# Kernel tuning notes

Measured on AMD Instinct MI355X. Metric: run time of the kernel, lower is better.

The kernel has to match this reference:

```python
import jax, jax.numpy as jnp
import numpy as np
from jax import lax

NS, C_IN, C_FEAT, CROP = 16, 3, 32, 256


def _conv(x, w, b):
    # 3x3 stride-1 'SAME' conv == padding=1 in torch
    y = lax.conv_general_dilated(x, w, (1, 1), 'SAME',
                                 dimension_numbers=('NCHW', 'OIHW', 'NCHW'))
    return y + b[None, :, None, None]


def _lrn(x, size=5, alpha=1e-4, beta=0.75, k=1.0):
    # PyTorch LocalResponseNorm: x / (k + alpha/size * sum_window x^2)^beta
    pad = size // 2
    sq = jnp.pad(x * x, ((0, 0), (pad, pad), (0, 0), (0, 0)))
    c = x.shape[1]
    win = sum(sq[:, i:i + c] for i in range(size))
    return x / (k + (alpha / size) * win) ** beta


def setup_inputs() -> dict:
    key = jax.random.key(0)
    ks = jax.random.split(key, 6)
    s = 0.05
    h = np.hanning(CROP).astype(np.float32)
    cos_window = jnp.asarray(np.outer(h, h))
    return {
        'z': jax.random.normal(ks[0], (NS, C_IN, CROP, CROP), jnp.float32),
        'w1': jax.random.normal(ks[1], (C_FEAT, C_IN, 3, 3), jnp.float32) * s,
        'b1': jax.random.normal(ks[2], (C_FEAT,), jnp.float32) * s,
        'w2': jax.random.normal(ks[3], (C_FEAT, C_FEAT, 3, 3), jnp.float32) * s,
        'b2': jax.random.normal(ks[4], (C_FEAT,), jnp.float32) * s,
        'cos_window': cos_window,
        'wf': jax.random.normal(ks[5], (1, C_FEAT, CROP, CROP // 2 + 1, 2), jnp.float32) * s,
    }


def reference(z, w1, b1, w2, b2, cos_window, wf):
    # feature extractor: conv -> relu -> conv -> LRN
    f = jax.nn.relu(_conv(z, w1, b1))
    f = _lrn(_conv(f, w2, b2))
    f = f * cos_window  # (ns, 32, crop, crop)
    zf = jnp.fft.rfft2(f, axes=(-2, -1))  # (ns, 32, crop, crop//2+1) complex
    # faithful to source: w_star = conj(wf), and the loop always uses w_star[0, 1]
    # (fixed channel 1) multiplied with zf[c, l], accumulated over l. wf is detached.
    wc = lax.stop_gradient(wf[0, 1, :, :, 0] - 1j * wf[0, 1, :, :, 1])
    ftrans = wc[None, None] * jnp.sum(zf, axis=1, keepdims=True)  # (ns,1,crop,crop//2+1)
    response = jnp.fft.irfft2(ftrans, s=(CROP, CROP), axes=(-2, -1))
    return response  # (ns, 1, crop, crop)
```

## Files before the change

kernel.cpp:

```cpp
#include <hip/hip_runtime.h>
#include <math.h>

#define NS   16
#define CIN  3
#define CF   32
#define CROP 256
#define KH   129

typedef _Float16 half8  __attribute__((ext_vector_type(8)));
typedef _Float16 half4v __attribute__((ext_vector_type(4)));
typedef _Float16 half2v __attribute__((ext_vector_type(2)));
typedef float    f32x4  __attribute__((ext_vector_type(4)));
typedef unsigned int u32x4 __attribute__((ext_vector_type(4)));

__device__ __forceinline__ half8 neg8(half8 v) {
    u32x4 u = __builtin_bit_cast(u32x4, v);
    u ^= (u32x4){0x80008000u, 0x80008000u, 0x80008000u, 0x80008000u};
    return __builtin_bit_cast(half8, u);
}

__device__ __forceinline__ int swz8(int b, int nb) {
    int q = nb >> 3, r = nb & 7;
    int x = b & 7, o = b >> 3;
    return (x < r ? x * (q + 1) : r * (q + 1) + (x - r) * q) + o;
}

#define X_OFF 0
#define Z_OFF 21504
#define LDS_BYTES 23904

__device__ __forceinline__ int xaddr(int q, int s) {
    return X_OFF + (q << 6) + ((s ^ ((q >> 1) & 3)) << 4);
}

__device__ __forceinline__ int pi_of(int co) {
    int h = co >> 3, j = co & 7;
    return (j < 4) ? (h * 4 + j) : (16 + h * 4 + j - 4);
}
__device__ __forceinline__ int cinv_of(int p) {
    int h = (p & 15) >> 2;
    int j = (p & 3) + ((p >= 16) ? 4 : 0);
    return h * 8 + j;
}

__device__ __forceinline__ void split_pair(float v0, float v1,
                                           half2v* hp, half2v* lp) {
    _Float16 h0 = (_Float16)v0, h1 = (_Float16)v1;
    *hp = (half2v){h0, h1};
    *lp = (half2v){(_Float16)(v0 - (float)h0), (_Float16)(v1 - (float)h1)};
}

__global__ __launch_bounds__(256)
void prep(const float* __restrict__ w1, const float* __restrict__ w2,
          _Float16* __restrict__ w1pk, _Float16* __restrict__ w2lin,
          _Float16* __restrict__ TAh, _Float16* __restrict__ TAl,
          _Float16* __restrict__ G1h, _Float16* __restrict__ G1l,
          _Float16* __restrict__ G3h, _Float16* __restrict__ G3l,
          _Float16* __restrict__ TCh, _Float16* __restrict__ TCl)
{
    const int bid = blockIdx.x, tid = threadIdx.x;

    if (bid >= 134) {
        int base = (bid - 134) * 4096;
        #pragma unroll
        for (int i = 0; i < 16; ++i) {
            int e = base + tid + i * 256;
            if (e < 9216) {
                int co = e / 288;
                int r  = e - co * 288;
                int ci = r / 9, k9 = r - ci * 9;
                w2lin[(k9 * 32 + pi_of(co)) * 32 + ci] = (_Float16)w2[e];
            } else if (e < 9344) {
                int t = e - 9216;
                int lane = t & 63;
                int p = (t >> 6) * 16 + (lane & 15);
                int c = cinv_of(p);
                #pragma unroll
                for (int j = 0; j < 8; ++j) {
                    int k = ((lane >> 4) << 3) + j;
                    w1pk[t * 8 + j] = (k < 27) ? (_Float16)w1[c * 27 + k]
                                               : (_Float16)0.f;
                }
            }
        }
        return;
    }

    __shared__ float cs[256], sn[256];
    {
        float s, c;
        sincosf(0.02454369260617025967f * (float)tid, &s, &c);
        cs[tid] = c; sn[tid] = s;
    }
    __syncthreads();

    if (bid < 34) {
        int base = bid * 1024 + tid;
        #pragma unroll
        for (int i = 0; i < 4; ++i) {
            int p = base + i * 256;
            int j0 = (p & 3) * 2, lane = (p >> 2) & 63, q = p >> 8;
            int nt = q % 17, ks = q / 17;
            int x0 = ks * 32 + ((lane >> 4) << 3) + j0;
            int c = nt * 16 + (lane & 15);
            float v0 = 0.f, v1 = 0.f;
            if (c <= 128) {
                v0 =  cs[(x0 * c) & 255];
                v1 =  cs[((x0 + 1) * c) & 255];
            } else if (c >= 136 && c <= 264) {
                int cc = c - 136;
                v0 = -sn[(x0 * cc) & 255];
                v1 = -sn[((x0 + 1) * cc) & 255];
            }
            half2v hv, lv; split_pair(v0, v1, &hv, &lv);
            ((half2v*)TAh)[p] = hv; ((half2v*)TAl)[p] = lv;
        }
    } else if (bid < 98) {
        int base = (bid - 34) * 1024 + tid;
        #pragma unroll
        for (int i = 0; i < 4; ++i) {
            int p = base + i * 256;
            int j0 = (p & 3) * 2, lane = (p >> 2) & 63, q = p >> 8;
            int nt = q & 15, ks = q >> 4;
            int kk0 = ks * 32 + ((lane >> 4) << 3) + j0;
            int m  = nt * 16 + (lane & 15);
            int part = kk0 >> 8;
            int y0 = kk0 & 255;
            int i0 = (y0 * m) & 255, i1 = ((y0 + 1) * m) & 255;
            float cv0 = cs[i0], s0 = sn[i0], cv1 = cs[i1], s1 = sn[i1];
            half2v hv, lv;
            float a0 = part ? s0 : cv0,  a1 = part ? s1 : cv1;
            split_pair(a0, a1, &hv, &lv);
            ((half2v*)G1h)[p] = hv; ((half2v*)G1l)[p] = lv;
            a0 = (part ? -s0 : cv0) * (1.f/256.f);
            a1 = (part ? -s1 : cv1) * (1.f/256.f);
            split_pair(a0, a1, &hv, &lv);
            ((half2v*)G3h)[p] = hv; ((half2v*)G3l)[p] = lv;
        }
    } else {
        int base = (bid - 98) * 1024 + tid;
        #pragma unroll
        for (int i = 0; i < 4; ++i) {
            int p = base + i * 256;
            int j0 = (p & 3) * 2, lane = (p >> 2) & 63, q = p >> 8;
            int nt = q & 15, ks = q >> 4;
            int kk0 = ks * 32 + ((lane >> 4) << 3) + j0;
            int x  = nt * 16 + (lane & 15);
            int part = (kk0 >= 144) ? 1 : 0;
            int k0 = kk0 - part * 144;
            float v0 = 0.f, v1 = 0.f;
            if (k0 <= 128) {
                float w0 = (k0 == 0 || k0 == 128) ? 1.f : 2.f;
                int ii = (k0 * x) & 255;
                v0 = (part ? -w0 * sn[ii] : w0 * cs[ii]) * (1.f/256.f);
            }
            int k1 = k0 + 1;
            if (k1 <= 128) {
                float w1w = (k1 == 0 || k1 == 128) ? 1.f : 2.f;
                int ii = (k1 * x) & 255;
                v1 = (part ? -w1w * sn[ii] : w1w * cs[ii]) * (1.f/256.f);
            }
            half2v hv, lv; split_pair(v0, v1, &hv, &lv);
            ((half2v*)TCh)[p] = hv; ((half2v*)TCl)[p] = lv;
        }
    }
}

__global__ __launch_bounds__(256, 5)
void fused_features(const float* __restrict__ z,
                    const _Float16* __restrict__ w1pk,
                    const float* __restrict__ b1,
                    const _Float16* __restrict__ w2lin,
                    const float* __restrict__ b2,
                    const float* __restrict__ cosw,
                    _Float16* __restrict__ g2h, _Float16* __restrict__ g2l)
{
    __shared__ __align__(16) unsigned char smem[LDS_BYTES];
    _Float16* ztile = (_Float16*)(smem + Z_OFF);

    const int tid  = threadIdx.x;
    const int lane = tid & 63;
    const int wv   = tid >> 6;
    const int l15  = lane & 15;
    const int lhi  = lane >> 4;

    const int n  = blockIdx.z;
    const int bx = blockIdx.x, by = blockIdx.y;
    const int fy0 = by * 16 - 1;
    const int fx0 = bx * 16 - 1;

    const int zy0 = by * 16 - 2;
    const int zx0 = bx * 16 - 2;
    for (int idx = tid; idx < CIN * 400; idx += 256) {
        int ci = idx / 400;
        int r  = idx - ci * 400;
        int yy = r / 20, xx = r - yy * 20;
        int gy = zy0 + yy, gx = zx0 + xx;
        float v = 0.0f;
        if ((unsigned)gy < CROP && (unsigned)gx < CROP)
            v = z[((n * CIN + ci) * CROP + gy) * CROP + gx];
        ztile[idx] = (_Float16)v;
    }

    half8 w1f0 = *(const half8*)(w1pk + lane * 8);
    half8 w1f1 = *(const half8*)(w1pk + 512 + lane * 8);
    float bias1v[2][4], bias2v[2][4];
    #pragma unroll
    for (int cg = 0; cg < 2; ++cg)
        #pragma unroll
        for (int r = 0; r < 4; ++r) {
            bias1v[cg][r] = b1[8 * lhi + 4 * cg + r];
            bias2v[cg][r] = b2[8 * lhi + 4 * cg + r];
        }

    int offs[8];
    #pragma unroll
    for (int j = 0; j < 8; ++j) {
        int k = lhi * 8 + j;
        int ci = k / 9, rr = k - ci * 9;
        int ky = rr / 3, kx = rr - ky * 3;
        offs[j] = (k < 27) ? (ci * 400 + ky * 20 + kx) : 0;
    }
    __syncthreads();

    const f32x4 zero4 = {0.f, 0.f, 0.f, 0.f};
    for (int t = wv; t < 21; t += 4) {
        int qp = t * 16 + l15;
        int qpc = qp < 324 ? qp : 323;
        int y = qpc / 18, x = qpc - y * 18;
        const _Float16* zb = ztile + y * 20 + x;
        half8 bfrag;
        #pragma unroll
        for (int j = 0; j < 8; ++j) bfrag[j] = zb[offs[j]];
        f32x4 d0 = __builtin_amdgcn_mfma_f32_16x16x32_f16(w1f0, bfrag, zero4, 0, 0, 0);
        f32x4 d1 = __builtin_amdgcn_mfma_f32_16x16x32_f16(w1f1, bfrag, zero4, 0, 0, 0);
        int gy = fy0 + y, gx = fx0 + x;
        bool ok = ((unsigned)gy < CROP) && ((unsigned)gx < CROP) && (qp < 324);
        half8 o8;
        #pragma unroll
        for (int r = 0; r < 4; ++r) {
            float v0 = ok ? fmaxf(d0[r] + bias1v[0][r], 0.f) : 0.f;
            float v1 = ok ? fmaxf(d1[r] + bias1v[1][r], 0.f) : 0.f;
            o8[r]     = (_Float16)v0;
            o8[4 + r] = (_Float16)v1;
        }
        *(half8*)(smem + xaddr(qp, lhi)) = o8;
    }
    __syncthreads();

    f32x4 acc[4][2];
    #pragma unroll
    for (int tt = 0; tt < 4; ++tt)
        #pragma unroll
        for (int cg = 0; cg < 2; ++cg)
            #pragma unroll
            for (int r = 0; r < 4; ++r)
                acc[tt][cg][r] = bias2v[cg][r];

    #pragma unroll
    for (int k9 = 0; k9 < 9; ++k9) {
        const int ky = k9 / 3, kx = k9 - 3 * ky;
        half8 af0 = *(const half8*)(w2lin + (k9 * 32 + l15)      * 32 + lhi * 8);
        half8 af1 = *(const half8*)(w2lin + (k9 * 32 + l15 + 16) * 32 + lhi * 8);
        #pragma unroll
        for (int tt = 0; tt < 4; ++tt) {
            int q = (wv * 4 + tt + ky) * 18 + l15 + kx;
            half8 bf = *(const half8*)(smem + xaddr(q, lhi));
            acc[tt][0] = __builtin_amdgcn_mfma_f32_16x16x32_f16(af0, bf, acc[tt][0], 0, 0, 0);
            acc[tt][1] = __builtin_amdgcn_mfma_f32_16x16x32_f16(af1, bf, acc[tt][1], 0, 0, 0);
        }
    }

    const bool bot = (lhi == 0), top = (lhi == 3);
    #pragma unroll
    for (int tt = 0; tt < 4; ++tt) {
        float aA0 = acc[tt][0][0], aA1 = acc[tt][0][1],
              aA2 = acc[tt][0][2], aA3 = acc[tt][0][3];
        float aB0 = acc[tt][1][0], aB1 = acc[tt][1][1],
              aB2 = acc[tt][1][2], aB3 = acc[tt][1][3];
        float sA0 = aA0 * aA0, sA1 = aA1 * aA1, sA2 = aA2 * aA2, sA3 = aA3 * aA3;
        float sB0 = aB0 * aB0, sB1 = aB1 * aB1, sB2 = aB2 * aB2, sB3 = aB3 * aB3;
        int up = (lane + 16) & 63, dn = (lane + 48) & 63;
        float em2 = __shfl(sB2, dn); em2 = bot ? 0.f : em2;
        float em1 = __shfl(sB3, dn); em1 = bot ? 0.f : em1;
        float ep8 = __shfl(sA0, up); ep8 = top ? 0.f : ep8;
        float ep9 = __shfl(sA1, up); ep9 = top ? 0.f : ep9;
        float s = 0.f, win = em2 + em1 + sA0 + sA1 + sA2;
        float t2, f;
        t2 = 2e-5f * win; f = fmaf(t2, fmaf(t2, 0.65625f, -0.75f), 1.0f);
        s = fmaf(aA0, f, s);  win += sA3 - em2;
        t2 = 2e-5f * win; f = fmaf(t2, fmaf(t2, 0.65625f, -0.75f), 1.0f);
        s = fmaf(aA1, f, s);  win += sB0 - em1;
        t2 = 2e-5f * win; f = fmaf(t2, fmaf(t2, 0.65625f, -0.75f), 1.0f);
        s = fmaf(aA2, f, s);  win += sB1 - sA0;
        t2 = 2e-5f * win; f = fmaf(t2, fmaf(t2, 0.65625f, -0.75f), 1.0f);
        s = fmaf(aA3, f, s);  win += sB2 - sA1;
        t2 = 2e-5f * win; f = fmaf(t2, fmaf(t2, 0.65625f, -0.75f), 1.0f);
        s = fmaf(aB0, f, s);  win += sB3 - sA2;
        t2 = 2e-5f * win; f = fmaf(t2, fmaf(t2, 0.65625f, -0.75f), 1.0f);
        s = fmaf(aB1, f, s);  win += ep8 - sA3;
        t2 = 2e-5f * win; f = fmaf(t2, fmaf(t2, 0.65625f, -0.75f), 1.0f);
        s = fmaf(aB2, f, s);  win += ep9 - sB0;
        t2 = 2e-5f * win; f = fmaf(t2, fmaf(t2, 0.65625f, -0.75f), 1.0f);
        s = fmaf(aB3, f, s);
        s += __shfl_xor(s, 16);
        s += __shfl_xor(s, 32);
        if (lhi == 0) {
            int gy = by * 16 + wv * 4 + tt, gx = bx * 16 + l15;
            float val = s * cosw[gy * CROP + gx];
            _Float16 h = (_Float16)val;
            int o = (n * CROP + gy) * CROP + gx;
            g2h[o] = h;
            g2l[o] = (_Float16)(val - (float)h);
        }
    }
}

__global__ __launch_bounds__(256, 4)
void fft_rows(const _Float16* __restrict__ g2h, const _Float16* __restrict__ g2l,
              const _Float16* __restrict__ TAh, const _Float16* __restrict__ TAl,
              _Float16* __restrict__ Zth, _Float16* __restrict__ Ztl)
{
    const int lane = threadIdx.x & 63;
    const int bsw = swz8(blockIdx.x, 1088);
    const int wu = bsw * 4 + (threadIdx.x >> 6);
    const int mt = wu / 17, nt = wu - mt * 17;
    const int l15 = lane & 15, lhi = lane >> 4;
    const int rowA = mt * 16 + l15;

    f32x4 a0 = {}, a1 = {}, a2 = {};
    #pragma unroll
    for (int ks = 0; ks < 8; ++ks) {
        const int ao = rowA * 256 + ks * 32 + lhi * 8;
        half8 Ah = *(const half8*)(g2h + ao);
        half8 Al = *(const half8*)(g2l + ao);
        const int bo = ((ks * 17 + nt) * 64 + lane) * 8;
        half8 Bh = *(const half8*)(TAh + bo);
        half8 Bl = *(const half8*)(TAl + bo);
        a0 = __builtin_amdgcn_mfma_f32_16x16x32_f16(Ah, Bh, a0, 0, 0, 0);
        a1 = __builtin_amdgcn_mfma_f32_16x16x32_f16(Ah, Bl, a1, 0, 0, 0);
        a2 = __builtin_amdgcn_mfma_f32_16x16x32_f16(Al, Bh, a2, 0, 0, 0);
    }
    f32x4 acc;
    #pragma unroll
    for (int r = 0; r < 4; ++r) acc[r] = a0[r] + a1[r] + a2[r];

    const int rowD = mt * 16 + lhi * 4;
    const int n = rowD >> 8, y = rowD & 255;
    int c = nt * 16 + l15;
    int row_k = -1, koff = 0;
    if (c <= 128)                  { row_k = c;       koff = 0;   }
    else if (c >= 136 && c <= 264) { row_k = c - 136; koff = 256; }
    if (row_k >= 0) {
        half4v hv, lv;
        #pragma unroll
        for (int r = 0; r < 4; ++r) {
            float v = acc[r];
            _Float16 h = (_Float16)v;
            hv[r] = h; lv[r] = (_Float16)(v - (float)h);
        }
        size_t o = (size_t)(n * 129 + row_k) * 512 + koff + y;
        *(half4v*)(Zth + o) = hv;
        *(half4v*)(Ztl + o) = lv;
    }
}

__global__ __launch_bounds__(256, 2)
void fft_cols_mul(const _Float16* __restrict__ Zth, const _Float16* __restrict__ Ztl,
                  const _Float16* __restrict__ G1h, const _Float16* __restrict__ G1l,
                  const float* __restrict__ wf,
                  _Float16* __restrict__ Ph, _Float16* __restrict__ Pl)
{
    const int lane = threadIdx.x & 63;
    const int bsw = swz8(blockIdx.x, 516);
    const int wu = bsw * 4 + (threadIdx.x >> 6);
    const int mt = wu >> 4, nt = wu & 15;
    const int l15 = lane & 15, lhi = lane >> 4;
    const int rowA = mt * 16 + l15;

    f32x4 r0 = {}, r1 = {}, r2 = {}, i0 = {}, i1 = {}, i2 = {};
    #pragma unroll
    for (int ks = 0; ks < 8; ++ks) {
        const int ao0 = rowA * 512 + ks * 32 + lhi * 8;
        half8 Ah0 = *(const half8*)(Zth + ao0);
        half8 Al0 = *(const half8*)(Ztl + ao0);
        half8 Ah1 = *(const half8*)(Zth + ao0 + 256);
        half8 Al1 = *(const half8*)(Ztl + ao0 + 256);
        const int bo0 = ((ks * 16 + nt) * 64 + lane) * 8;
        half8 B0h = *(const half8*)(G1h + bo0);
        half8 B0l = *(const half8*)(G1l + bo0);
        half8 B1h_ = *(const half8*)(G1h + bo0 + 65536);
        half8 B1l_ = *(const half8*)(G1l + bo0 + 65536);
        half8 nB1h = neg8(B1h_), nB1l = neg8(B1l_);
        r0 = __builtin_amdgcn_mfma_f32_16x16x32_f16(Ah0, B0h,  r0, 0, 0, 0);
        r1 = __builtin_amdgcn_mfma_f32_16x16x32_f16(Ah0, B0l,  r1, 0, 0, 0);
        r2 = __builtin_amdgcn_mfma_f32_16x16x32_f16(Al0, B0h,  r2, 0, 0, 0);
        r0 = __builtin_amdgcn_mfma_f32_16x16x32_f16(Ah1, B1h_, r0, 0, 0, 0);
        r1 = __builtin_amdgcn_mfma_f32_16x16x32_f16(Ah1, B1l_, r1, 0, 0, 0);
        r2 = __builtin_amdgcn_mfma_f32_16x16x32_f16(Al1, B1h_, r2, 0, 0, 0);
        i0 = __builtin_amdgcn_mfma_f32_16x16x32_f16(Ah0, nB1h, i0, 0, 0, 0);
        i1 = __builtin_amdgcn_mfma_f32_16x16x32_f16(Ah0, nB1l, i1, 0, 0, 0);
        i2 = __builtin_amdgcn_mfma_f32_16x16x32_f16(Al0, nB1h, i2, 0, 0, 0);
        i0 = __builtin_amdgcn_mfma_f32_16x16x32_f16(Ah1, B0h,  i0, 0, 0, 0);
        i1 = __builtin_amdgcn_mfma_f32_16x16x32_f16(Ah1, B0l,  i1, 0, 0, 0);
        i2 = __builtin_amdgcn_mfma_f32_16x16x32_f16(Al1, B0h,  i2, 0, 0, 0);
    }
    const int rowP0 = mt * 16 + lhi * 4;
    const int m = nt * 16 + l15;
    const float* wf1 = wf + 256 * 129 * 2;
    int n_ = rowP0 / 129;
    int k_ = rowP0 - n_ * 129;
    #pragma unroll
    for (int r = 0; r < 4; ++r) {
        float wr = wf1[(m * 129 + k_) * 2 + 0];
        float wi = wf1[(m * 129 + k_) * 2 + 1];
        float fr = r0[r] + r1[r] + r2[r];
        float fi = i0[r] + i1[r] + i2[r];
        float pr = wr * fr + wi * fi;
        float pi = wr * fi - wi * fr;
        size_t o = (size_t)(rowP0 + r) * 512 + m;
        _Float16 h;
        h = (_Float16)pr; Ph[o] = h;       Pl[o] = (_Float16)(pr - (float)h);
        h = (_Float16)pi; Ph[o + 256] = h; Pl[o + 256] = (_Float16)(pi - (float)h);
        if (++k_ == 129) { k_ = 0; ++n_; }
    }
}

__global__ __launch_bounds__(256, 2)
void fft_cols_inv(const _Float16* __restrict__ Ph, const _Float16* __restrict__ Pl,
                  const _Float16* __restrict__ G3h, const _Float16* __restrict__ G3l,
                  _Float16* __restrict__ Bth, _Float16* __restrict__ Btl)
{
    const int lane = threadIdx.x & 63;
    const int bsw = swz8(blockIdx.x, 516);
    const int wu = bsw * 4 + (threadIdx.x >> 6);
    const int mt = wu >> 4, nt = wu & 15;
    const int l15 = lane & 15, lhi = lane >> 4;
    const int rowA = mt * 16 + l15;

    f32x4 r0 = {}, r1 = {}, r2 = {}, i0 = {}, i1 = {}, i2 = {};
    #pragma unroll
    for (int ks = 0; ks < 8; ++ks) {
        const int ao0 = rowA * 512 + ks * 32 + lhi * 8;
        half8 Ah0 = *(const half8*)(Ph + ao0);
        half8 Al0 = *(const half8*)(Pl + ao0);
        half8 Ah1 = *(const half8*)(Ph + ao0 + 256);
        half8 Al1 = *(const half8*)(Pl + ao0 + 256);
        const int bo0 = ((ks * 16 + nt) * 64 + lane) * 8;
        half8 B0h = *(const half8*)(G3h + bo0);
        half8 B0l = *(const half8*)(G3l + bo0);
        half8 B1h_ = *(const half8*)(G3h + bo0 + 65536);
        half8 B1l_ = *(const half8*)(G3l + bo0 + 65536);
        half8 nB1h = neg8(B1h_), nB1l = neg8(B1l_);
        r0 = __builtin_amdgcn_mfma_f32_16x16x32_f16(Ah0, B0h,  r0, 0, 0, 0);
        r1 = __builtin_amdgcn_mfma_f32_16x16x32_f16(Ah0, B0l,  r1, 0, 0, 0);
        r2 = __builtin_amdgcn_mfma_f32_16x16x32_f16(Al0, B0h,  r2, 0, 0, 0);
        r0 = __builtin_amdgcn_mfma_f32_16x16x32_f16(Ah1, B1h_, r0, 0, 0, 0);
        r1 = __builtin_amdgcn_mfma_f32_16x16x32_f16(Ah1, B1l_, r1, 0, 0, 0);
        r2 = __builtin_amdgcn_mfma_f32_16x16x32_f16(Al1, B1h_, r2, 0, 0, 0);
        i0 = __builtin_amdgcn_mfma_f32_16x16x32_f16(Ah0, nB1h, i0, 0, 0, 0);
        i1 = __builtin_amdgcn_mfma_f32_16x16x32_f16(Ah0, nB1l, i1, 0, 0, 0);
        i2 = __builtin_amdgcn_mfma_f32_16x16x32_f16(Al0, nB1h, i2, 0, 0, 0);
        i0 = __builtin_amdgcn_mfma_f32_16x16x32_f16(Ah1, B0h,  i0, 0, 0, 0);
        i1 = __builtin_amdgcn_mfma_f32_16x16x32_f16(Ah1, B0l,  i1, 0, 0, 0);
        i2 = __builtin_amdgcn_mfma_f32_16x16x32_f16(Al1, B0h,  i2, 0, 0, 0);
    }
    const int rowP0 = mt * 16 + lhi * 4;
    const int y = nt * 16 + l15;
    int n_ = rowP0 / 129;
    int k_ = rowP0 - n_ * 129;
    #pragma unroll
    for (int r = 0; r < 4; ++r) {
        size_t base = (size_t)(n_ * 256 + y) * 288 + k_;
        float v = r0[r] + r1[r] + r2[r];
        _Float16 h = (_Float16)v;
        Bth[base] = h;  Btl[base] = (_Float16)(v - (float)h);
        float v2 = i0[r] + i1[r] + i2[r];
        _Float16 h2 = (_Float16)v2;
        Bth[base + 144] = h2;  Btl[base + 144] = (_Float16)(v2 - (float)h2);
        if (++k_ == 129) { k_ = 0; ++n_; }
    }
}

__global__ __launch_bounds__(256, 4)
void irfft_rows(const _Float16* __restrict__ Bth, const _Float16* __restrict__ Btl,
                const _Float16* __restrict__ TCh, const _Float16* __restrict__ TCl,
                float* __restrict__ out)
{
    const int lane = threadIdx.x & 63;
    const int bsw = swz8(blockIdx.x, 1024);
    const int wu = bsw * 4 + (threadIdx.x >> 6);
    const int mt = wu >> 4, nt = wu & 15;
    const int l15 = lane & 15, lhi = lane >> 4;
    const int rowA = mt * 16 + l15;

    f32x4 a0 = {}, a1 = {}, a2 = {};
    #pragma unroll
    for (int ks = 0; ks < 9; ++ks) {
        const int ao = rowA * 288 + ks * 32 + lhi * 8;
        half8 Ah = *(const half8*)(Bth + ao);
        half8 Al = *(const half8*)(Btl + ao);
        const int bo = ((ks * 16 + nt) * 64 + lane) * 8;
        half8 Bh = *(const half8*)(TCh + bo);
        half8 Bl = *(const half8*)(TCl + bo);
        a0 = __builtin_amdgcn_mfma_f32_16x16x32_f16(Ah, Bh, a0, 0, 0, 0);
        a1 = __builtin_amdgcn_mfma_f32_16x16x32_f16(Ah, Bl, a1, 0, 0, 0);
        a2 = __builtin_amdgcn_mfma_f32_16x16x32_f16(Al, Bh, a2, 0, 0, 0);
    }
    const int rowD = mt * 16 + lhi * 4;
    const int x = nt * 16 + l15;
    #pragma unroll
    for (int r = 0; r < 4; ++r)
        out[(size_t)(rowD + r) * 256 + x] = a0[r] + a1[r] + a2[r];
}

extern "C" void kernel_launch(void* const* d_in, const int* in_sizes, int n_in,
                              void* d_out, int out_size, void* d_ws, size_t ws_size,
                              hipStream_t stream)
{
    const float* z    = (const float*)d_in[0];
    const float* w1   = (const float*)d_in[1];
    const float* b1   = (const float*)d_in[2];
    const float* w2   = (const float*)d_in[3];
    const float* b2   = (const float*)d_in[4];
    const float* cosw = (const float*)d_in[5];
    const float* wf   = (const float*)d_in[6];
    float* out = (float*)d_out;

    char* p = (char*)d_ws;
    auto take = [&](size_t bytes) {
        char* r = p; p += (bytes + 255) & ~(size_t)255; return r;
    };
    _Float16* g2h = (_Float16*)take(4096 * 256 * 2);
    _Float16* g2l = (_Float16*)take(4096 * 256 * 2);
    _Float16* Zth = (_Float16*)take(2064 * 512 * 2);
    _Float16* Ztl = (_Float16*)take(2064 * 512 * 2);
    _Float16* Ph  = (_Float16*)take(2064 * 512 * 2);
    _Float16* Pl  = (_Float16*)take(2064 * 512 * 2);
    _Float16* Bth = (_Float16*)take(4096 * 288 * 2);
    _Float16* Btl = (_Float16*)take(4096 * 288 * 2);
    _Float16* TAh = (_Float16*)take(69632 * 2);
    _Float16* TAl = (_Float16*)take(69632 * 2);
    _Float16* G1h = (_Float16*)take(131072 * 2);
    _Float16* G1l = (_Float16*)take(131072 * 2);
    _Float16* G3h = (_Float16*)take(131072 * 2);
    _Float16* G3l = (_Float16*)take(131072 * 2);
    _Float16* TCh = (_Float16*)take(73728 * 2);
    _Float16* TCl = (_Float16*)take(73728 * 2);
    _Float16* w1pk  = (_Float16*)take(1024 * 2);
    _Float16* w2lin = (_Float16*)take(9216 * 2);

    prep<<<137, 256, 0, stream>>>(w1, w2, w1pk, w2lin, TAh, TAl,
                                  G1h, G1l, G3h, G3l, TCh, TCl);
    fused_features<<<dim3(16, 16, NS), 256, 0, stream>>>(z, w1pk, b1, w2lin, b2,
                                                         cosw, g2h, g2l);
    fft_rows<<<1088, 256, 0, stream>>>(g2h, g2l, TAh, TAl, Zth, Ztl);
    fft_cols_mul<<<516, 256, 0, stream>>>(Zth, Ztl, G1h, G1l, wf, Ph, Pl);
    fft_cols_inv<<<516, 256, 0, stream>>>(Ph, Pl, G3h, G3l, Bth, Btl);
    irfft_rows<<<1024, 256, 0, stream>>>(Bth, Btl, TCh, TCl, out);
}
```

Measured before the change: 110.6 us.

## Split K across wave pairs in FFT GEMM kernels with LDS reduction

Each output tile of the four DFT-as-GEMM kernels is now computed by two waves, each covering half of the K dimension. The second wave writes its partial accumulators to shared memory and the first wave adds them before the epilogue, so twice as many blocks are launched. The aim is more waves in flight and shorter dependent MFMA chains, hiding memory latency. It costs a block barrier, an LDS round trip and idle half-blocks during the epilogue; occupancy hints were also raised, including for the feature kernel.

```diff
diff --git a/kernel.cpp b/kernel.cpp
--- a/kernel.cpp
+++ b/kernel.cpp
@@ -166,7 +166,7 @@
     }
 }
 
-__global__ __launch_bounds__(256, 5)
+__global__ __launch_bounds__(256, 6)
 void fused_features(const float* __restrict__ z,
                     const _Float16* __restrict__ w1pk,
                     const float* __restrict__ b1,
@@ -321,16 +321,20 @@
               const _Float16* __restrict__ TAh, const _Float16* __restrict__ TAl,
               _Float16* __restrict__ Zth, _Float16* __restrict__ Ztl)
 {
+    __shared__ f32x4 part[2][3][64];
     const int lane = threadIdx.x & 63;
-    const int bsw = swz8(blockIdx.x, 1088);
-    const int wu = bsw * 4 + (threadIdx.x >> 6);
-    const int mt = wu / 17, nt = wu - mt * 17;
+    const int w = threadIdx.x >> 6;
+    const int u = w >> 1, kh = w & 1;
+    const int bsw = swz8(blockIdx.x, 2176);
+    const int unit = bsw * 2 + u;
+    const int mt = unit / 17, nt = unit - mt * 17;
     const int l15 = lane & 15, lhi = lane >> 4;
     const int rowA = mt * 16 + l15;
 
     f32x4 a0 = {}, a1 = {}, a2 = {};
     #pragma unroll
-    for (int ks = 0; ks < 8; ++ks) {
+    for (int i = 0; i < 4; ++i) {
+        const int ks = kh * 4 + i;
         const int ao = rowA * 256 + ks * 32 + lhi * 8;
         half8 Ah = *(const half8*)(g2h + ao);
         half8 Al = *(const half8*)(g2l + ao);
@@ -341,6 +345,13 @@
         a1 = __builtin_amdgcn_mfma_f32_16x16x32_f16(Ah, Bl, a1, 0, 0, 0);
         a2 = __builtin_amdgcn_mfma_f32_16x16x32_f16(Al, Bh, a2, 0, 0, 0);
     }
+    if (kh) {
+        part[u][0][lane] = a0; part[u][1][lane] = a1; part[u][2][lane] = a2;
+    }
+    __syncthreads();
+    if (kh) return;
+    a0 += part[u][0][lane]; a1 += part[u][1][lane]; a2 += part[u][2][lane];
+
     f32x4 acc;
     #pragma unroll
     for (int r = 0; r < 4; ++r) acc[r] = a0[r] + a1[r] + a2[r];
@@ -365,22 +376,26 @@
     }
 }
 
-__global__ __launch_bounds__(256, 2)
+__global__ __launch_bounds__(256, 4)
 void fft_cols_mul(const _Float16* __restrict__ Zth, const _Float16* __restrict__ Ztl,
                   const _Float16* __restrict__ G1h, const _Float16* __restrict__ G1l,
                   const float* __restrict__ wf,
                   _Float16* __restrict__ Ph, _Float16* __restrict__ Pl)
 {
+    __shared__ f32x4 part[2][6][64];
     const int lane = threadIdx.x & 63;
-    const int bsw = swz8(blockIdx.x, 516);
-    const int wu = bsw * 4 + (threadIdx.x >> 6);
-    const int mt = wu >> 4, nt = wu & 15;
+    const int w = threadIdx.x >> 6;
+    const int u = w >> 1, kh = w & 1;
+    const int bsw = swz8(blockIdx.x, 1032);
+    const int unit = bsw * 2 + u;
+    const int mt = unit >> 4, nt = unit & 15;
     const int l15 = lane & 15, lhi = lane >> 4;
     const int rowA = mt * 16 + l15;
 
     f32x4 r0 = {}, r1 = {}, r2 = {}, i0 = {}, i1 = {}, i2 = {};
     #pragma unroll
-    for (int ks = 0; ks < 8; ++ks) {
+    for (int i = 0; i < 4; ++i) {
+        const int ks = kh * 4 + i;
         const int ao0 = rowA * 512 + ks * 32 + lhi * 8;
         half8 Ah0 = *(const half8*)(Zth + ao0);
         half8 Al0 = *(const half8*)(Ztl + ao0);
@@ -405,6 +420,15 @@
         i1 = __builtin_amdgcn_mfma_f32_16x16x32_f16(Ah1, B0l,  i1, 0, 0, 0);
         i2 = __builtin_amdgcn_mfma_f32_16x16x32_f16(Al1, B0h,  i2, 0, 0, 0);
     }
+    if (kh) {
+        part[u][0][lane] = r0; part[u][1][lane] = r1; part[u][2][lane] = r2;
+        part[u][3][lane] = i0; part[u][4][lane] = i1; part[u][5][lane] = i2;
+    }
+    __syncthreads();
+    if (kh) return;
+    r0 += part[u][0][lane]; r1 += part[u][1][lane]; r2 += part[u][2][lane];
+    i0 += part[u][3][lane]; i1 += part[u][4][lane]; i2 += part[u][5][lane];
+
     const int rowP0 = mt * 16 + lhi * 4;
     const int m = nt * 16 + l15;
     const float* wf1 = wf + 256 * 129 * 2;
@@ -426,21 +450,25 @@
     }
 }
 
-__global__ __launch_bounds__(256, 2)
+__global__ __launch_bounds__(256, 4)
 void fft_cols_inv(const _Float16* __restrict__ Ph, const _Float16* __restrict__ Pl,
                   const _Float16* __restrict__ G3h, const _Float16* __restrict__ G3l,
                   _Float16* __restrict__ Bth, _Float16* __restrict__ Btl)
 {
+    __shared__ f32x4 part[2][6][64];
     const int lane = threadIdx.x & 63;
-    const int bsw = swz8(blockIdx.x, 516);
-    const int wu = bsw * 4 + (threadIdx.x >> 6);
-    const int mt = wu >> 4, nt = wu & 15;
+    const int w = threadIdx.x >> 6;
+    const int u = w >> 1, kh = w & 1;
+    const int bsw = swz8(blockIdx.x, 1032);
+    const int unit = bsw * 2 + u;
+    const int mt = unit >> 4, nt = unit & 15;
     const int l15 = lane & 15, lhi = lane >> 4;
     const int rowA = mt * 16 + l15;
 
     f32x4 r0 = {}, r1 = {}, r2 = {}, i0 = {}, i1 = {}, i2 = {};
     #pragma unroll
-    for (int ks = 0; ks < 8; ++ks) {
+    for (int i = 0; i < 4; ++i) {
+        const int ks = kh * 4 + i;
         const int ao0 = rowA * 512 + ks * 32 + lhi * 8;
         half8 Ah0 = *(const half8*)(Ph + ao0);
         half8 Al0 = *(const half8*)(Pl + ao0);
@@ -465,6 +493,15 @@
         i1 = __builtin_amdgcn_mfma_f32_16x16x32_f16(Ah1, B0l,  i1, 0, 0, 0);
         i2 = __builtin_amdgcn_mfma_f32_16x16x32_f16(Al1, B0h,  i2, 0, 0, 0);
     }
+    if (kh) {
+        part[u][0][lane] = r0; part[u][1][lane] = r1; part[u][2][lane] = r2;
+        part[u][3][lane] = i0; part[u][4][lane] = i1; part[u][5][lane] = i2;
+    }
+    __syncthreads();
+    if (kh) return;
+    r0 += part[u][0][lane]; r1 += part[u][1][lane]; r2 += part[u][2][lane];
+    i0 += part[u][3][lane]; i1 += part[u][4][lane]; i2 += part[u][5][lane];
+
     const int rowP0 = mt * 16 + lhi * 4;
     const int y = nt * 16 + l15;
     int n_ = rowP0 / 129;
@@ -487,16 +524,21 @@
                 const _Float16* __restrict__ TCh, const _Float16* __restrict__ TCl,
                 float* __restrict__ out)
 {
+    __shared__ f32x4 part[2][3][64];
     const int lane = threadIdx.x & 63;
-    const int bsw = swz8(blockIdx.x, 1024);
-    const int wu = bsw * 4 + (threadIdx.x >> 6);
-    const int mt = wu >> 4, nt = wu & 15;
+    const int w = threadIdx.x >> 6;
+    const int u = w >> 1, kh = w & 1;
+    const int bsw = swz8(blockIdx.x, 2048);
+    const int unit = bsw * 2 + u;
+    const int mt = unit >> 4, nt = unit & 15;
     const int l15 = lane & 15, lhi = lane >> 4;
     const int rowA = mt * 16 + l15;
 
     f32x4 a0 = {}, a1 = {}, a2 = {};
     #pragma unroll
-    for (int ks = 0; ks < 9; ++ks) {
+    for (int i = 0; i < 5; ++i) {
+        if (kh && i == 4) break;
+        const int ks = kh * 5 + i;
         const int ao = rowA * 288 + ks * 32 + lhi * 8;
         half8 Ah = *(const half8*)(Bth + ao);
         half8 Al = *(const half8*)(Btl + ao);
@@ -507,6 +549,13 @@
         a1 = __builtin_amdgcn_mfma_f32_16x16x32_f16(Ah, Bl, a1, 0, 0, 0);
         a2 = __builtin_amdgcn_mfma_f32_16x16x32_f16(Al, Bh, a2, 0, 0, 0);
     }
+    if (kh) {
+        part[u][0][lane] = a0; part[u][1][lane] = a1; part[u][2][lane] = a2;
+    }
+    __syncthreads();
+    if (kh) return;
+    a0 += part[u][0][lane]; a1 += part[u][1][lane]; a2 += part[u][2][lane];
+
     const int rowD = mt * 16 + lhi * 4;
     const int x = nt * 16 + l15;
     #pragma unroll
@@ -554,8 +603,8 @@
                                   G1h, G1l, G3h, G3l, TCh, TCl);
     fused_features<<<dim3(16, 16, NS), 256, 0, stream>>>(z, w1pk, b1, w2lin, b2,
                                                          cosw, g2h, g2l);
-    fft_rows<<<1088, 256, 0, stream>>>(g2h, g2l, TAh, TAl, Zth, Ztl);
-    fft_cols_mul<<<516, 256, 0, stream>>>(Zth, Ztl, G1h, G1l, wf, Ph, Pl);
-    fft_cols_inv<<<516, 256, 0, stream>>>(Ph, Pl, G3h, G3l, Bth, Btl);
-    irfft_rows<<<1024, 256, 0, stream>>>(Bth, Btl, TCh, TCl, out);
-}
+    fft_rows<<<2176, 256, 0, stream>>>(g2h, g2l, TAh, TAl, Zth, Ztl);
+    fft_cols_mul<<<1032, 256, 0, stream>>>(Zth, Ztl, G1h, G1l, wf, Ph, Pl);
+    fft_cols_inv<<<1032, 256, 0, stream>>>(Ph, Pl, G3h, G3l, Bth, Btl);
+    irfft_rows<<<2048, 256, 0, stream>>>(Bth, Btl, TCh, TCl, out);
+}
```

Result: slower. 138.9 us (+25.6%).
